# Kernel optimization log

Hardware: AMD Instinct MI355X
Metric: run time of the kernel (lower is better)

Reference implementation:

```python
import jax, jax.numpy as jnp
import numpy as np

HEAD_SIZE = 64

def setup_inputs() -> dict:
    key = jax.random.key(0)
    ks = jax.random.split(key, 6)
    B, T, C = 4, 4096, 1024
    H = HEAD_SIZE
    return {
        "q": jax.random.normal(ks[0], (B, T, C), dtype=jnp.float32),
        "k": jax.random.normal(ks[1], (B, T, C), dtype=jnp.float32),
        "v": jax.random.normal(ks[2], (B, T, C), dtype=jnp.float32),
        "Wq": jax.random.normal(ks[3], (H, C), dtype=jnp.float32) * (C ** -0.5),
        "Wk": jax.random.normal(ks[4], (H, C), dtype=jnp.float32) * (C ** -0.5),
        "Wv": jax.random.normal(ks[5], (H, C), dtype=jnp.float32) * (C ** -0.5),
    }

def reference(q, k, v, Wq, Wk, Wv):
    # dropout p=0.0 -> identity (module applies F.dropout before each projection)
    T = q.shape[1]
    scale = HEAD_SIZE ** -0.5
    Q = jnp.einsum('btc,hc->bth', q, Wq)   # [B,T,H]
    K = jnp.einsum('btc,hc->bth', k, Wk)   # [B,T,H]
    V = jnp.einsum('btc,hc->bth', v, Wv)   # [B,T,H]
    scores = jnp.einsum('bth,bsh->bts', Q, K) * scale  # [B,T,T]
    # non-standard mask: tril with diagonal=1 (each query sees positions <= i+1)
    mask = jnp.tril(jnp.ones((T, T), dtype=bool), k=1)
    scores = jnp.where(mask, scores, -jnp.inf)
    # double scaling as in the original: softmax(scores * head_size**-0.5)
    weights = jax.nn.softmax(scores * scale, axis=-1)
    return jnp.einsum('bts,bsh->bth', weights, V)
```

## Files before the change

### kernel.cpp

```cpp
#include <hip/hip_runtime.h>
#include <hip/hip_bf16.h>

#define BB 4
#define TT 4096
#define CC 1024
#define HH 64

typedef _Float16 f16;
typedef __attribute__((ext_vector_type(8))) _Float16 f16x8;
typedef __attribute__((ext_vector_type(4))) _Float16 f16x4;
typedef __attribute__((ext_vector_type(4))) float f32x4;

#define MFMA32(a,b,c) __builtin_amdgcn_mfma_f32_16x16x32_f16((a),(b),(c),0,0,0)
#define MFMA16(a,b,c) __builtin_amdgcn_mfma_f32_16x16x16f16((a),(b),(c),0,0,0)

#define WF_ELEMS (3 * 32 * 4 * 64 * 8)
#define CHUNK_F16 1024
#define PB_F16 (256 * CHUNK_F16)

static __device__ __forceinline__ void gl_lds16(const void* g, void* l) {
  __builtin_amdgcn_global_load_lds(
      (const __attribute__((address_space(1))) unsigned int*)g,
      (__attribute__((address_space(3))) unsigned int*)l, 16, 0, 0);
}

static __device__ __forceinline__ f16x8 pack2(f32x4 a, f32x4 b) {
  f16x8 r;
  r[0]=(f16)a[0]; r[1]=(f16)a[1]; r[2]=(f16)a[2]; r[3]=(f16)a[3];
  r[4]=(f16)b[0]; r[5]=(f16)b[1]; r[6]=(f16)b[2]; r[7]=(f16)b[3];
  return r;
}

__global__ __launch_bounds__(64) void wrepack_kernel(
    const float* __restrict__ Wqg, const float* __restrict__ Wkg,
    const float* __restrict__ Wvg, f16* __restrict__ Wf)
{
  const int bx = blockIdx.x;
  const int nt = bx & 3;
  const int kc = (bx >> 2) & 31;
  const int p  = bx >> 7;
  const float* W = (p == 0) ? Wqg : (p == 1) ? Wkg : Wvg;
  const float sc = (p == 0) ? (1.4426950408889634f / 64.0f) : 1.0f;

  const int lane = threadIdx.x;
  const int l16 = lane & 15, quad = lane >> 4;
  const float* src = W + (size_t)(nt * 16 + l16) * CC + kc * 32 + quad * 8;
  f32x4 a = *(const f32x4*)src;
  f32x4 b = *(const f32x4*)(src + 4);
  f16x8 r;
  #pragma unroll
  for (int j = 0; j < 4; ++j) { r[j] = (f16)(a[j] * sc); r[j + 4] = (f16)(b[j] * sc); }
  *(f16x8*)(Wf + (size_t)bx * 512 + lane * 8) = r;
}

__global__ __launch_bounds__(256) void proj_kernel(
    const float* __restrict__ qg, const float* __restrict__ kg, const float* __restrict__ vg,
    const f16* __restrict__ Wf,
    f16* __restrict__ Qf, f16* __restrict__ Kf, f16* __restrict__ Vf)
{
  __shared__ float Xs[2][64][64];
  __shared__ f16   Ws[2][8][64][8];

  const float* X; f16* O; const int p = blockIdx.y;
  if (p == 0)      { X = qg; O = Qf; }
  else if (p == 1) { X = kg; O = Kf; }
  else             { X = vg; O = Vf; }

  const int tid  = threadIdx.x;
  const int w    = tid >> 6;
  const int lane = tid & 63;
  const int quad = lane >> 4;
  const int l16  = lane & 15;
  const int r0   = blockIdx.x * 64;

  const float* Xrow[4];
  #pragma unroll
  for (int s = 0; s < 4; ++s) {
    const int R  = w * 16 + s * 4 + (lane >> 4);
    const int lc = (lane & 15) ^ ((R & 7) << 1);
    Xrow[s] = X + (size_t)(r0 + R) * CC + lc * 4;
  }
  const f16* Wfp = Wf + (size_t)p * 128 * 512;
  const f16* Wsrc[2];
  #pragma unroll
  for (int jj = 0; jj < 2; ++jj)
    Wsrc[jj] = Wfp + (size_t)(2 * w + jj) * 512 + lane * 8;

  f32x4 acc[4];
  #pragma unroll
  for (int nt = 0; nt < 4; ++nt) acc[nt] = (f32x4){0.f, 0.f, 0.f, 0.f};

  #pragma unroll
  for (int s = 0; s < 4; ++s)
    gl_lds16(Xrow[s], &Xs[0][w * 16 + s * 4][0]);
  #pragma unroll
  for (int jj = 0; jj < 2; ++jj)
    gl_lds16(Wsrc[jj], &Ws[0][2 * w + jj][0][0]);

  const int sw = (l16 & 7) << 1;

  for (int it = 0; it < 16; ++it) {
    const int buf = it & 1;
    __syncthreads();
    if (it < 15) {
      #pragma unroll
      for (int s = 0; s < 4; ++s)
        gl_lds16(Xrow[s] + (it + 1) * 64, &Xs[buf ^ 1][w * 16 + s * 4][0]);
      #pragma unroll
      for (int jj = 0; jj < 2; ++jj)
        gl_lds16(Wsrc[jj] + (size_t)(it + 1) * 4096, &Ws[buf ^ 1][2 * w + jj][0][0]);
    }
    #pragma unroll
    for (int kk = 0; kk < 2; ++kk) {
      const int c0 = kk * 8 + quad * 2;
      f32x4 a0 = *(const f32x4*)&Xs[buf][w * 16 + l16][(c0 ^ sw) * 4];
      f32x4 a1 = *(const f32x4*)&Xs[buf][w * 16 + l16][((c0 + 1) ^ sw) * 4];
      f16x8 af = pack2(a0, a1);
      #pragma unroll
      for (int nt = 0; nt < 4; ++nt) {
        f16x8 bf = *(const f16x8*)&Ws[buf][kk * 4 + nt][lane][0];
        acc[nt] = MFMA32(af, bf, acc[nt]);
      }
    }
  }

  f16 (*Ls)[66] = (f16(*)[66])&Xs[0][w * 16][0];
  #pragma unroll
  for (int nt = 0; nt < 4; ++nt)
    #pragma unroll
    for (int r = 0; r < 4; ++r)
      Ls[quad * 4 + r][nt * 16 + l16] = (f16)acc[nt][r];
  const size_t chunk = (size_t)blockIdx.x * 4 + w;
  if (p < 2) {
    #pragma unroll
    for (int h = 0; h < 2; ++h) {
      f16x8 t = *(const f16x8*)&Ls[l16][h * 32 + quad * 8];
      *(f16x8*)(O + (chunk * 2 + h) * 512 + lane * 8) = t;
    }
  } else {
    #pragma unroll
    for (int np = 0; np < 2; ++np) {
      f16x8 t;
      #pragma unroll
      for (int j = 0; j < 8; ++j)
        t[j] = Ls[quad * 4 + (j & 3)][(2 * np + (j >> 2)) * 16 + l16];
      *(f16x8*)(O + (chunk * 2 + np) * 512 + lane * 8) = t;
    }
  }
}

__device__ __forceinline__ void attn_tile(
    int b, int j, int a, int e, int wave, int quad, int l16, int lane, int sp,
    const f16* __restrict__ Qf, const f16* __restrict__ Kf, const f16* __restrict__ Vf,
    f16 (*Ks)[8][64][8], f16 (*Vs)[8][64][8],
    float* __restrict__ Opart, float* __restrict__ lpart)
{
  const int m0 = j * 64 + wave * 16;

  const f16* Kfb = Kf + (size_t)b * PB_F16;
  const f16* Vfb = Vf + (size_t)b * PB_F16;
  const f16* Qfb = Qf + (size_t)b * PB_F16;

  f16x8 qa0 = *(const f16x8*)(Qfb + ((size_t)(m0 >> 4) * 2 + 0) * 512 + lane * 8);
  f16x8 qa1 = *(const f16x8*)(Qfb + ((size_t)(m0 >> 4) * 2 + 1) * 512 + lane * 8);

  f32x4 o[4];
  float lsum = 0.f;
  #pragma unroll
  for (int nt = 0; nt < 4; ++nt) o[nt] = (f32x4){0.f, 0.f, 0.f, 0.f};

  __syncthreads();

  if (a < e) {
    #pragma unroll
    for (int jj = 0; jj < 2; ++jj) {
      const int idx = 2 * wave + jj;
      gl_lds16(Kfb + (size_t)a * 4096 + idx * 512 + lane * 8, &Ks[0][idx][0][0]);
      gl_lds16(Vfb + (size_t)a * 4096 + idx * 512 + lane * 8, &Vs[0][idx][0][0]);
    }
  }

  for (int st = a; st < e; ++st) {
    const int buf = (st - a) & 1;
    __syncthreads();
    if (st + 1 < e) {
      #pragma unroll
      for (int jj = 0; jj < 2; ++jj) {
        const int idx = 2 * wave + jj;
        gl_lds16(Kfb + (size_t)(st + 1) * 4096 + idx * 512 + lane * 8, &Ks[buf ^ 1][idx][0][0]);
        gl_lds16(Vfb + (size_t)(st + 1) * 4096 + idx * 512 + lane * 8, &Vs[buf ^ 1][idx][0][0]);
      }
    }
    const int s0 = st * 64;

    f32x4 sc[4];
    #pragma unroll
    for (int ct = 0; ct < 4; ++ct) {
      f16x8 k0 = *(const f16x8*)&Ks[buf][ct * 2][lane][0];
      f16x8 k1 = *(const f16x8*)&Ks[buf][ct * 2 + 1][lane][0];
      f32x4 z = (f32x4){0.f, 0.f, 0.f, 0.f};
      z = MFMA32(k0, qa0, z);
      sc[ct] = MFMA32(k1, qa1, z);
    }

    const bool domask = (s0 + 63) > (m0 + 1);
    f16x4 pa[4];
    #pragma unroll
    for (int ct = 0; ct < 4; ++ct) {
      #pragma unroll
      for (int r = 0; r < 4; ++r) {
        float x = sc[ct][r];
        if (domask) {
          const int key = s0 + ct * 16 + quad * 4 + r;
          if (key > m0 + l16 + 1) x = -__builtin_inff();
        }
        const float pv = __builtin_amdgcn_exp2f(x);
        lsum += pv;
        pa[ct][r] = (f16)pv;
      }
    }

    #pragma unroll
    for (int ct = 0; ct < 4; ++ct) {
      #pragma unroll
      for (int np = 0; np < 2; ++np) {
        f16x8 vv = *(const f16x8*)&Vs[buf][ct * 2 + np][lane][0];
        f16x4 blo = __builtin_shufflevector(vv, vv, 0, 1, 2, 3);
        f16x4 bhi = __builtin_shufflevector(vv, vv, 4, 5, 6, 7);
        o[2 * np]     = MFMA16(pa[ct], blo, o[2 * np]);
        o[2 * np + 1] = MFMA16(pa[ct], bhi, o[2 * np + 1]);
      }
    }
  }

  lsum += __shfl_xor(lsum, 16, 64);
  lsum += __shfl_xor(lsum, 32, 64);
  const size_t rbase = (size_t)(sp * BB + b) * TT;
  if (quad == 0) lpart[rbase + m0 + l16] = lsum;
  #pragma unroll
  for (int nt = 0; nt < 4; ++nt)
    #pragma unroll
    for (int r = 0; r < 4; ++r)
      Opart[(rbase + m0 + quad * 4 + r) * HH + nt * 16 + l16] = o[nt][r];
}

__global__ __launch_bounds__(256) void attn_kernel(
    const f16* __restrict__ Qf, const f16* __restrict__ Kf, const f16* __restrict__ Vf,
    float* __restrict__ Opart, float* __restrict__ lpart, int S)
{
  __shared__ f16 Ks[2][8][64][8];
  __shared__ f16 Vs[2][8][64][8];

  const int pr = blockIdx.x;
  const int sp = blockIdx.y;
  const int b  = blockIdx.z;
  const int tid  = threadIdx.x;
  const int wave = tid >> 6;
  const int lane = tid & 63;
  const int quad = lane >> 4;
  const int l16  = lane & 15;

  const int j1 = pr, j2 = 63 - pr;
  const int n1 = min(j1 + 2, 64), n2 = min(j2 + 2, 64);
  const int tot = n1 + n2;
  const int lo = tot * sp / S, hi = tot * (sp + 1) / S;
  const int a1 = min(lo, n1), e1 = min(hi, n1);
  const int a2 = max(lo - n1, 0), e2 = max(hi - n1, 0);

  attn_tile(b, j1, a1, e1, wave, quad, l16, lane, sp, Qf, Kf, Vf, Ks, Vs, Opart, lpart);
  attn_tile(b, j2, a2, e2, wave, quad, l16, lane, sp, Qf, Kf, Vf, Ks, Vs, Opart, lpart);
}

__global__ __launch_bounds__(256) void combine_kernel(
    const float* __restrict__ Opart, const float* __restrict__ lpart,
    float* __restrict__ out, int S)
{
  const int idx = blockIdx.x * 256 + threadIdx.x;
  const int row = idx >> 4;
  const int c   = (idx & 15) * 4;
  float l = 0.f;
  f32x4 s = (f32x4){0.f, 0.f, 0.f, 0.f};
  for (int p = 0; p < S; ++p) {
    l += lpart[(size_t)p * BB * TT + row];
    s += *(const f32x4*)&Opart[((size_t)p * BB * TT + row) * HH + c];
  }
  const float inv = 1.0f / l;
  *(f32x4*)&out[(size_t)row * HH + c] = s * inv;
}

extern "C" void kernel_launch(void* const* d_in, const int* in_sizes, int n_in,
                              void* d_out, int out_size, void* d_ws, size_t ws_size,
                              hipStream_t stream)
{
  const float* q  = (const float*)d_in[0];
  const float* k  = (const float*)d_in[1];
  const float* v  = (const float*)d_in[2];
  const float* Wq = (const float*)d_in[3];
  const float* Wk = (const float*)d_in[4];
  const float* Wv = (const float*)d_in[5];
  float* out = (float*)d_out;

  const size_t n = (size_t)BB * TT * HH;
  const size_t need8 = (WF_ELEMS + 3 * n) * sizeof(f16)
                     + 8 * n * sizeof(float) + 8 * (size_t)BB * TT * sizeof(float);
  const int S = (ws_size >= need8) ? 8 : 4;

  f16* Wf = (f16*)d_ws;
  f16* Qf = Wf + WF_ELEMS;
  f16* Kf = Qf + n;
  f16* Vf = Kf + n;
  float* Opart = (float*)(Vf + n);
  float* lpart = Opart + (size_t)S * n;

  wrepack_kernel<<<dim3(384), 64, 0, stream>>>(Wq, Wk, Wv, Wf);
  proj_kernel<<<dim3(256, 3), 256, 0, stream>>>(q, k, v, Wf, Qf, Kf, Vf);
  attn_kernel<<<dim3(32, S, BB), 256, 0, stream>>>(Qf, Kf, Vf, Opart, lpart, S);
  combine_kernel<<<dim3(1024), 256, 0, stream>>>(Opart, lpart, out, S);
}
```

Before: 236.2 us.

## Load projection operands directly from global memory instead of LDS double-buffering

Replaces the LDS double-buffered pipeline (global_load_lds into swizzled X and W tiles, with a barrier every iteration) with direct per-lane global vector loads of X rows and pre-packed W fragments, fully unrolled over 32 K-chunks. This removes the block-level __syncthreads and the LDS staging traffic, and shrinks shared memory to a small per-wave output staging buffer, which may raise occupancy. The trade-off is that W fragments are re-read from global/L2 by every wave, and latency hiding now depends on the compiler hoisting loads in the unrolled loop rather than on explicit prefetch.

```diff
diff --git a/kernel.cpp b/kernel.cpp
--- a/kernel.cpp
+++ b/kernel.cpp
@@ -58,8 +58,7 @@
     const f16* __restrict__ Wf,
     f16* __restrict__ Qf, f16* __restrict__ Kf, f16* __restrict__ Vf)
 {
-  __shared__ float Xs[2][64][64];
-  __shared__ f16   Ws[2][8][64][8];
+  __shared__ f16 Lsw[4][16][66];
 
   const float* X; f16* O; const int p = blockIdx.y;
   if (p == 0)      { X = qg; O = Qf; }
@@ -71,60 +70,28 @@
   const int lane = tid & 63;
   const int quad = lane >> 4;
   const int l16  = lane & 15;
-  const int r0   = blockIdx.x * 64;
-
-  const float* Xrow[4];
-  #pragma unroll
-  for (int s = 0; s < 4; ++s) {
-    const int R  = w * 16 + s * 4 + (lane >> 4);
-    const int lc = (lane & 15) ^ ((R & 7) << 1);
-    Xrow[s] = X + (size_t)(r0 + R) * CC + lc * 4;
-  }
-  const f16* Wfp = Wf + (size_t)p * 128 * 512;
-  const f16* Wsrc[2];
-  #pragma unroll
-  for (int jj = 0; jj < 2; ++jj)
-    Wsrc[jj] = Wfp + (size_t)(2 * w + jj) * 512 + lane * 8;
+  const int r0   = blockIdx.x * 64 + w * 16;
+
+  const float* xrow = X + (size_t)(r0 + l16) * CC + quad * 8;
+  const f16* wbase = Wf + (size_t)p * 128 * 512 + lane * 8;
 
   f32x4 acc[4];
   #pragma unroll
   for (int nt = 0; nt < 4; ++nt) acc[nt] = (f32x4){0.f, 0.f, 0.f, 0.f};
 
   #pragma unroll
-  for (int s = 0; s < 4; ++s)
-    gl_lds16(Xrow[s], &Xs[0][w * 16 + s * 4][0]);
-  #pragma unroll
-  for (int jj = 0; jj < 2; ++jj)
-    gl_lds16(Wsrc[jj], &Ws[0][2 * w + jj][0][0]);
-
-  const int sw = (l16 & 7) << 1;
-
-  for (int it = 0; it < 16; ++it) {
-    const int buf = it & 1;
-    __syncthreads();
-    if (it < 15) {
-      #pragma unroll
-      for (int s = 0; s < 4; ++s)
-        gl_lds16(Xrow[s] + (it + 1) * 64, &Xs[buf ^ 1][w * 16 + s * 4][0]);
-      #pragma unroll
-      for (int jj = 0; jj < 2; ++jj)
-        gl_lds16(Wsrc[jj] + (size_t)(it + 1) * 4096, &Ws[buf ^ 1][2 * w + jj][0][0]);
-    }
-    #pragma unroll
-    for (int kk = 0; kk < 2; ++kk) {
-      const int c0 = kk * 8 + quad * 2;
-      f32x4 a0 = *(const f32x4*)&Xs[buf][w * 16 + l16][(c0 ^ sw) * 4];
-      f32x4 a1 = *(const f32x4*)&Xs[buf][w * 16 + l16][((c0 + 1) ^ sw) * 4];
-      f16x8 af = pack2(a0, a1);
-      #pragma unroll
-      for (int nt = 0; nt < 4; ++nt) {
-        f16x8 bf = *(const f16x8*)&Ws[buf][kk * 4 + nt][lane][0];
-        acc[nt] = MFMA32(af, bf, acc[nt]);
-      }
-    }
-  }
-
-  f16 (*Ls)[66] = (f16(*)[66])&Xs[0][w * 16][0];
+  for (int kc = 0; kc < 32; ++kc) {
+    f32x4 a0 = *(const f32x4*)(xrow + kc * 32);
+    f32x4 a1 = *(const f32x4*)(xrow + kc * 32 + 4);
+    f16x8 af = pack2(a0, a1);
+    #pragma unroll
+    for (int nt = 0; nt < 4; ++nt) {
+      f16x8 bf = *(const f16x8*)(wbase + ((size_t)kc * 4 + nt) * 512);
+      acc[nt] = MFMA32(af, bf, acc[nt]);
+    }
+  }
+
+  f16 (*Ls)[66] = Lsw[w];
   #pragma unroll
   for (int nt = 0; nt < 4; ++nt)
     #pragma unroll
```

Result: slower. 242.3 us (+2.6%).
